# Kernel tuning notes

Hardware: AMD Instinct MI355X
Metric: run time of the kernel (lower is better)

## Reference

```python
import jax, jax.numpy as jnp
import numpy as np

# ---- config (matches init_kwargs) ----
CLIP_FRAMES, CLIP_STRIDE = 1, 2
CODEBOOK_SIZE, CODEBOOK_DIM = 1024, 512
WORD_SIZE = CODEBOOK_SIZE // 4
VOCAB = 3000
LAMBDA_MMD, LAMBDA_SIM = 0.1, 1.0


def conv3d(x, w, b, pad):
    # x: (N,C,T,H,W), w: (O,I,kt,kh,kw)
    out = jax.lax.conv_general_dilated(x, w, (1, 1, 1), [(p, p) for p in pad],
                                       dimension_numbers=('NCDHW', 'OIDHW', 'NCDHW'))
    return out + b[None, :, None, None, None]


def bn_relu(x, g, b, nc):
    # training-mode BatchNorm3d, stats computed per clip-batch (over B,T,H,W),
    # matching the torch loop that calls the encoder once per clip.
    s = x.shape
    xr = x.reshape((nc, s[0] // nc) + s[1:])
    m = xr.mean(axis=(1, 3, 4, 5), keepdims=True)
    v = xr.var(axis=(1, 3, 4, 5), keepdims=True)
    xn = (xr - m) * jax.lax.rsqrt(v + 1e-5)
    xn = xn * g[None, None, :, None, None, None] + b[None, None, :, None, None, None]
    return jax.nn.relu(xn).reshape(s)


def maxpool_hw(x):
    return jax.lax.reduce_window(x, -jnp.inf, jax.lax.max,
                                 (1, 1, 1, 2, 2), (1, 1, 1, 2, 2), 'VALID')


def gru_layer(x, w_ih, w_hh, b_ih, b_hh):
    # PyTorch GRU cell math; x: (B,L,D) -> (B,L,H)
    B = x.shape[0]
    H = w_hh.shape[1]

    def step(h, xt):
        gi = xt @ w_ih.T + b_ih
        gh = h @ w_hh.T + b_hh
        i_r, i_z, i_n = jnp.split(gi, 3, axis=-1)
        h_r, h_z, h_n = jnp.split(gh, 3, axis=-1)
        r = jax.nn.sigmoid(i_r + h_r)
        z = jax.nn.sigmoid(i_z + h_z)
        n = jnp.tanh(i_n + r * h_n)
        hn = (1.0 - z) * n + z * h
        return hn, hn

    h0 = jnp.zeros((B, H), x.dtype)
    _, ys = jax.lax.scan(step, h0, jnp.swapaxes(x, 0, 1))
    return jnp.swapaxes(ys, 0, 1)


def nearest_code(flat, book):
    # squared euclidean distance; argmin identical to torch.cdist(p=2)+argmin
    d2 = (flat * flat).sum(-1, keepdims=True) - 2.0 * flat @ book.T + (book * book).sum(-1)
    return jnp.argmin(d2, axis=-1)


def _forward(videos, conv1_w, conv1_b, bn1_g, bn1_b, conv2_w, conv2_b, bn2_g, bn2_b,
             conv3_w, conv3_b, bn3_g, bn3_b, tconv_w, tconv_b, bn4_g, bn4_b,
             proj_w, proj_b, codebook, word_codebook, align_w, align_b,
             gru_wih0, gru_whh0, gru_bih0, gru_bhh0, gru_wih1, gru_whh1, gru_bih1, gru_bhh1,
             dec1_w, dec1_b, dec2_w, dec2_b, dec3_w, dec3_b, text_tokens):
    sg = jax.lax.stop_gradient
    B, _, T, Hh, Ww = videos.shape
    nc = (T - CLIP_FRAMES) // CLIP_STRIDE + 1
    # gather all clips, fold clip dim into batch for the convs
    idx = jnp.arange(nc)[:, None] * CLIP_STRIDE + jnp.arange(CLIP_FRAMES)[None]
    clips = jnp.transpose(videos[:, :, idx], (2, 0, 1, 3, 4, 5))  # (nc,B,3,cf,H,W)
    x = clips.reshape(nc * B, 3, CLIP_FRAMES, Hh, Ww)
    x = maxpool_hw(bn_relu(conv3d(x, conv1_w, conv1_b, (1, 1, 1)), bn1_g, bn1_b, nc))
    x = maxpool_hw(bn_relu(conv3d(x, conv2_w, conv2_b, (1, 1, 1)), bn2_g, bn2_b, nc))
    x = bn_relu(conv3d(x, conv3_w, conv3_b, (1, 1, 1)), bn3_g, bn3_b, nc)
    # AdaptiveAvgPool3d((CLIP_FRAMES,4,4)): T already CLIP_FRAMES, H,W divisible by 4
    N, C, Tc, Hc, Wc = x.shape
    x = x.reshape(N, C, Tc, 4, Hc // 4, 4, Wc // 4).mean(axis=(4, 6))
    x = bn_relu(conv3d(x, tconv_w, tconv_b, (1, 0, 0)), bn4_g, bn4_b, nc)
    feats = jnp.transpose(x.reshape(nc, B, -1), (1, 0, 2))  # (B, nc, 256*cf*16)
    features = feats @ proj_w.T + proj_b                     # (B, nc, D)
    D = features.shape[-1]
    # --- VQ quantize ---
    flat = features.reshape(-1, D)
    tok = nearest_code(flat, codebook)
    quantized = codebook[tok].reshape(B, nc, D)
    commitment = jnp.mean((features - sg(quantized)) ** 2)
    codebook_loss = jnp.mean((quantized - sg(features)) ** 2)
    h = gru_layer(quantized[:, :-1], gru_wih0, gru_whh0, gru_bih0, gru_bhh0)
    h = gru_layer(h, gru_wih1, gru_whh1, gru_bih1, gru_bhh1)
    context_loss = jnp.mean((h - features[:, 1:]) ** 2)
    vq_loss = commitment + 0.25 * codebook_loss + 0.1 * context_loss
    # --- SimpleCRA: mean of char pairs -> nearest word code ---
    wsrc = quantized.reshape(B, nc // 2, 2, D).mean(axis=2)
    widx = nearest_code(wsrc.reshape(-1, D), word_codebook).reshape(B, nc // 2)
    wemb = word_codebook[widx]  # (B, nw, D)
    flat_w = wemb.reshape(-1, D)
    alignment = jnp.mean((flat_w @ align_w.T + align_b - sg(flat_w)) ** 2)
    # --- translation: mean word context -> MLP decoder -> CE vs first token, summed over batch ---
    ctx = wemb.mean(axis=1)  # (B, D)
    hh = jax.nn.relu(ctx @ dec1_w.T + dec1_b)
    hh = jax.nn.relu(hh @ dec2_w.T + dec2_b)  # dropout = identity (eval)
    logits = hh @ dec3_w.T + dec3_b           # (B, VOCAB)
    logp = jax.nn.log_softmax(logits, axis=-1)
    translation = -jnp.take_along_axis(logp, text_tokens[:, :1], axis=1).sum()
    total = vq_loss + LAMBDA_MMD * alignment + LAMBDA_SIM * translation
    return widx, total


def setup_inputs() -> dict:
    key = jax.random.key(0)
    ks = iter(jax.random.split(key, 48))

    def rn(shape, scale):
        return jax.random.normal(next(ks), shape, jnp.float32) * scale

    D = CODEBOOK_DIM
    inp = {}
    inp['videos'] = jax.random.normal(next(ks), (4, 3, 32, 64, 64), jnp.float32)
    inp['conv1_w'] = rn((64, 3, 3, 3, 3), 0.15); inp['conv1_b'] = jnp.zeros((64,), jnp.float32)
    inp['bn1_g'] = jnp.ones((64,), jnp.float32); inp['bn1_b'] = jnp.zeros((64,), jnp.float32)
    inp['conv2_w'] = rn((128, 64, 3, 3, 3), 0.034); inp['conv2_b'] = jnp.zeros((128,), jnp.float32)
    inp['bn2_g'] = jnp.ones((128,), jnp.float32); inp['bn2_b'] = jnp.zeros((128,), jnp.float32)
    inp['conv3_w'] = rn((256, 128, 3, 3, 3), 0.024); inp['conv3_b'] = jnp.zeros((256,), jnp.float32)
    inp['bn3_g'] = jnp.ones((256,), jnp.float32); inp['bn3_b'] = jnp.zeros((256,), jnp.float32)
    inp['tconv_w'] = rn((256, 256, 3, 1, 1), 0.05); inp['tconv_b'] = jnp.zeros((256,), jnp.float32)
    inp['bn4_g'] = jnp.ones((256,), jnp.float32); inp['bn4_b'] = jnp.zeros((256,), jnp.float32)
    inp['proj_w'] = rn((D, 256 * CLIP_FRAMES * 16), 0.02); inp['proj_b'] = jnp.zeros((D,), jnp.float32)
    inp['codebook'] = jax.random.uniform(next(ks), (CODEBOOK_SIZE, D), jnp.float32,
                                         -1.0 / CODEBOOK_SIZE, 1.0 / CODEBOOK_SIZE)
    inp['word_codebook'] = jax.random.uniform(next(ks), (WORD_SIZE, D), jnp.float32,
                                              -1.0 / WORD_SIZE, 1.0 / WORD_SIZE)
    inp['align_w'] = rn((D, D), 0.04); inp['align_b'] = jnp.zeros((D,), jnp.float32)
    for l in (0, 1):
        inp[f'gru_wih{l}'] = rn((3 * D, D), 0.044)
        inp[f'gru_whh{l}'] = rn((3 * D, D), 0.044)
        inp[f'gru_bih{l}'] = jnp.zeros((3 * D,), jnp.float32)
        inp[f'gru_bhh{l}'] = jnp.zeros((3 * D,), jnp.float32)
    inp['dec1_w'] = rn((512, D), 0.044); inp['dec1_b'] = jnp.zeros((512,), jnp.float32)
    inp['dec2_w'] = rn((1024, 512), 0.044); inp['dec2_b'] = jnp.zeros((1024,), jnp.float32)
    inp['dec3_w'] = rn((VOCAB, 1024), 0.031); inp['dec3_b'] = jnp.zeros((VOCAB,), jnp.float32)
    inp['text_tokens'] = jax.random.randint(next(ks), (4, 10), 0, VOCAB)
    return inp


def reference(videos, conv1_w, conv1_b, bn1_g, bn1_b, conv2_w, conv2_b, bn2_g, bn2_b,
              conv3_w, conv3_b, bn3_g, bn3_b, tconv_w, tconv_b, bn4_g, bn4_b,
              proj_w, proj_b, codebook, word_codebook, align_w, align_b,
              gru_wih0, gru_whh0, gru_bih0, gru_bhh0, gru_wih1, gru_whh1, gru_bih1, gru_bhh1,
              dec1_w, dec1_b, dec2_w, dec2_b, dec3_w, dec3_b, text_tokens):
    return _forward(videos, conv1_w, conv1_b, bn1_g, bn1_b, conv2_w, conv2_b, bn2_g, bn2_b,
                    conv3_w, conv3_b, bn3_g, bn3_b, tconv_w, tconv_b, bn4_g, bn4_b,
                    proj_w, proj_b, codebook, word_codebook, align_w, align_b,
                    gru_wih0, gru_whh0, gru_bih0, gru_bhh0, gru_wih1, gru_whh1, gru_bih1, gru_bhh1,
                    dec1_w, dec1_b, dec2_w, dec2_b, dec3_w, dec3_b, text_tokens)
```

## Files before the change

### kernel.cpp

```cpp
#include <hip/hip_runtime.h>


static const size_t OFF_X1P  = 0;
static const size_t OFF_Y2   = 4194304;
static const size_t OFF_X2P  = 0;
static const size_t OFF_Y3   = 4194304;
static const size_t OFF_X3P  = 2097152;
static const size_t OFF_Y4   = 2359296;
static const size_t OFF_X4   = 2621440;
static const size_t OFF_FEAT = 2883584;
static const size_t OFF_QUANT= 2916352;
static const size_t OFF_GI1  = 2949120;
static const size_t OFF_GI2  = 3047424;
static const size_t OFF_H1   = 3145728;
static const size_t OFF_H2   = 3178496;
static const size_t OFF_WEMB = 3211264;
static const size_t OFF_CTX  = 3227648;
static const size_t OFF_HH1  = 3229696;
static const size_t OFF_HH2  = 3231744;
static const size_t OFF_LOG  = 3235840;
static const size_t OFF_PP   = 3247840;
static const size_t OFF_SC    = 12582912;
static const size_t OFF_SH    = 12587008;
static const size_t OFF_ACCP  = 12591104;
static const size_t OFF_COMMIT= 12623872;
static const size_t OFF_CTXA  = 12623936;
static const size_t OFF_ALIGNA= 12624056;

__global__ __launch_bounds__(256) void k_conv1_stats3(
        const float* __restrict__ videos, const float* __restrict__ w1,
        const float* __restrict__ b1, float* __restrict__ accP) {
    __shared__ float sP[3 * 18 * 66];
    __shared__ float wsm[3 * 9 * 16];
    __shared__ float sRed[4][16], qRed[4][16];
    int oc0 = blockIdx.x * 16, rq = blockIdx.y, n = blockIdx.z;
    int c = n >> 2, b = n & 3;
    int tid = threadIdx.x;
    int rp = tid >> 5, cq = tid & 31;
    for (int e = tid; e < 3564; e += 256) {
        int ic = e / 1188, rem = e % 1188;
        int r = rem / 66, col = rem % 66;
        int gr = rq * 16 - 1 + r, gc = col - 1;
        float v = 0.f;
        if (gr >= 0 && gr < 64 && gc >= 0 && gc < 64)
            v = videos[((size_t)(b * 3 + ic) * 32 + 2 * c) * 4096 + gr * 64 + gc];
        sP[e] = v;
    }
    for (int e = tid; e < 432; e += 256) {
        int ic = e / 144, rem = e % 144, k = rem / 16, j = rem % 16;
        wsm[e] = w1[((size_t)((oc0 + j) * 3 + ic) * 3 + 1) * 9 + k];
    }
    __syncthreads();
    float acc[4][16];
#pragma unroll
    for (int p = 0; p < 4; ++p)
#pragma unroll
        for (int j = 0; j < 16; ++j) acc[p][j] = 0.f;
#pragma unroll
    for (int ic = 0; ic < 3; ++ic) {
        const float* base = &sP[ic * 1188 + (2 * rp) * 66 + 2 * cq];
        float patch[4][4];
#pragma unroll
        for (int r = 0; r < 4; ++r)
#pragma unroll
            for (int q = 0; q < 4; ++q) patch[r][q] = base[r * 66 + q];
#pragma unroll
        for (int k = 0; k < 9; ++k) {
            int kr = k / 3, kc = k % 3;
            float4 w0 = *(const float4*)&wsm[(ic * 9 + k) * 16 + 0];
            float4 w1v = *(const float4*)&wsm[(ic * 9 + k) * 16 + 4];
            float4 w2 = *(const float4*)&wsm[(ic * 9 + k) * 16 + 8];
            float4 w3 = *(const float4*)&wsm[(ic * 9 + k) * 16 + 12];
#pragma unroll
            for (int p = 0; p < 4; ++p) {
                float vv = patch[(p >> 1) + kr][(p & 1) + kc];
                acc[p][0]  += vv * w0.x; acc[p][1]  += vv * w0.y;
                acc[p][2]  += vv * w0.z; acc[p][3]  += vv * w0.w;
                acc[p][4]  += vv * w1v.x; acc[p][5]  += vv * w1v.y;
                acc[p][6]  += vv * w1v.z; acc[p][7]  += vv * w1v.w;
                acc[p][8]  += vv * w2.x; acc[p][9]  += vv * w2.y;
                acc[p][10] += vv * w2.z; acc[p][11] += vv * w2.w;
                acc[p][12] += vv * w3.x; acc[p][13] += vv * w3.y;
                acc[p][14] += vv * w3.z; acc[p][15] += vv * w3.w;
            }
        }
    }
    int lane = tid & 63, wave = tid >> 6;
#pragma unroll
    for (int j = 0; j < 16; ++j) {
        float bj = b1[oc0 + j];
        float s = 0.f, q = 0.f;
#pragma unroll
        for (int p = 0; p < 4; ++p) {
            float a = acc[p][j] + bj;
            s += a; q += a * a;
        }
#pragma unroll
        for (int m = 1; m < 64; m <<= 1) {
            s += __shfl_xor(s, m);
            q += __shfl_xor(q, m);
        }
        if (lane == 0) { sRed[wave][j] = s; qRed[wave][j] = q; }
    }
    __syncthreads();
    if (tid < 16) {
        float s = ((sRed[0][tid] + sRed[1][tid]) + (sRed[2][tid] + sRed[3][tid]));
        float q = ((qRed[0][tid] + qRed[1][tid]) + (qRed[2][tid] + qRed[3][tid]));
        int oc = oc0 + tid;
        size_t slot = (((size_t)(c * 64 + oc)) * 4 + b) * 4 + rq;
        accP[slot] = s;
        accP[16384 + slot] = q;
    }
}

__global__ void k_conv1_fin(const float* __restrict__ accP, const float* __restrict__ g1,
                            const float* __restrict__ be1, float* __restrict__ sc,
                            float* __restrict__ sh) {
    int e = blockIdx.x * 256 + threadIdx.x;
    if (e >= 1024) return;
    int oc = e & 63;
    const float* ps = accP + (size_t)e * 16;
    const float* pq = accP + 16384 + (size_t)e * 16;
    float s = 0.f, q = 0.f;
#pragma unroll
    for (int i = 0; i < 16; ++i) { s += ps[i]; q += pq[i]; }
    float m = s * (1.f / 16384.f);
    float var = q * (1.f / 16384.f) - m * m;
    float sf = g1[oc] * rsqrtf(var + 1e-5f);
    sc[e] = sf;
    sh[e] = be1[oc] - m * sf;
}

__global__ __launch_bounds__(256) void k_conv1_apply3(
        const float* __restrict__ videos, const float* __restrict__ w1,
        const float* __restrict__ b1, const float* __restrict__ sc,
        const float* __restrict__ sh, float* __restrict__ x1p) {
    __shared__ float sP[3 * 18 * 66];
    __shared__ float wsm[3 * 9 * 16];
    int oc0 = blockIdx.x * 16, rq = blockIdx.y, n = blockIdx.z;
    int c = n >> 2, b = n & 3;
    int tid = threadIdx.x;
    int rp = tid >> 5, cq = tid & 31;
    for (int e = tid; e < 3564; e += 256) {
        int ic = e / 1188, rem = e % 1188;
        int r = rem / 66, col = rem % 66;
        int gr = rq * 16 - 1 + r, gc = col - 1;
        float v = 0.f;
        if (gr >= 0 && gr < 64 && gc >= 0 && gc < 64)
            v = videos[((size_t)(b * 3 + ic) * 32 + 2 * c) * 4096 + gr * 64 + gc];
        sP[e] = v;
    }
    for (int e = tid; e < 432; e += 256) {
        int ic = e / 144, rem = e % 144, k = rem / 16, j = rem % 16;
        wsm[e] = w1[((size_t)((oc0 + j) * 3 + ic) * 3 + 1) * 9 + k];
    }
    __syncthreads();
    float acc[4][16];
#pragma unroll
    for (int p = 0; p < 4; ++p)
#pragma unroll
        for (int j = 0; j < 16; ++j) acc[p][j] = 0.f;
#pragma unroll
    for (int ic = 0; ic < 3; ++ic) {
        const float* base = &sP[ic * 1188 + (2 * rp) * 66 + 2 * cq];
        float patch[4][4];
#pragma unroll
        for (int r = 0; r < 4; ++r)
#pragma unroll
            for (int q = 0; q < 4; ++q) patch[r][q] = base[r * 66 + q];
#pragma unroll
        for (int k = 0; k < 9; ++k) {
            int kr = k / 3, kc = k % 3;
            float4 w0 = *(const float4*)&wsm[(ic * 9 + k) * 16 + 0];
            float4 w1v = *(const float4*)&wsm[(ic * 9 + k) * 16 + 4];
            float4 w2 = *(const float4*)&wsm[(ic * 9 + k) * 16 + 8];
            float4 w3 = *(const float4*)&wsm[(ic * 9 + k) * 16 + 12];
#pragma unroll
            for (int p = 0; p < 4; ++p) {
                float vv = patch[(p >> 1) + kr][(p & 1) + kc];
                acc[p][0]  += vv * w0.x; acc[p][1]  += vv * w0.y;
                acc[p][2]  += vv * w0.z; acc[p][3]  += vv * w0.w;
                acc[p][4]  += vv * w1v.x; acc[p][5]  += vv * w1v.y;
                acc[p][6]  += vv * w1v.z; acc[p][7]  += vv * w1v.w;
                acc[p][8]  += vv * w2.x; acc[p][9]  += vv * w2.y;
                acc[p][10] += vv * w2.z; acc[p][11] += vv * w2.w;
                acc[p][12] += vv * w3.x; acc[p][13] += vv * w3.y;
                acc[p][14] += vv * w3.z; acc[p][15] += vv * w3.w;
            }
        }
    }
#pragma unroll
    for (int j = 0; j < 16; ++j) {
        int oc = oc0 + j;
        float bj = b1[oc];
        float scj = sc[c * 64 + oc], shj = sh[c * 64 + oc];
        float m = -1e30f;
#pragma unroll
        for (int p = 0; p < 4; ++p) m = fmaxf(m, (acc[p][j] + bj) * scj + shj);
        x1p[((size_t)n * 64 + oc) * 1024 + (rq * 8 + rp) * 32 + cq] = fmaxf(m, 0.f);
    }
}

__global__ __launch_bounds__(256) void k_conv2(
        const float* __restrict__ in, const float* __restrict__ wt,
        const float* __restrict__ bias, float* __restrict__ out) {
    __shared__ __align__(16) float sIn[8 * 10 * 36];
    __shared__ __align__(16) float sW[8 * 9 * 32];
    int oc0 = blockIdx.x * 32, r0 = blockIdx.y * 8, n = blockIdx.z;
    int tid = threadIdx.x;
    int ocq = tid >> 5;
    int rg = (tid >> 3) & 3;
    int cg = tid & 7;
    float acc[4][8];
#pragma unroll
    for (int j = 0; j < 4; ++j)
#pragma unroll
        for (int p = 0; p < 8; ++p) acc[j][p] = 0.f;

    for (int ic0 = 0; ic0 < 64; ic0 += 8) {
        __syncthreads();
        for (int e = tid; e < 2720; e += 256) {
            int ch = e / 340, rem = e % 340;
            int r = rem / 34, col = rem % 34;
            int gr = r0 - 1 + r, gc = col - 1;
            float v = 0.f;
            if (gr >= 0 && gr < 32 && gc >= 0 && gc < 32)
                v = in[((size_t)(n * 64 + ic0 + ch) * 32 + gr) * 32 + gc];
            sIn[ch * 360 + r * 36 + col] = v;
        }
        for (int e = tid; e < 2304; e += 256) {
            int c = e / 288, r1 = e % 288, k = r1 / 32, j = r1 % 32;
            sW[e] = wt[((size_t)(oc0 + j) * 64 + ic0 + c) * 27 + 9 + k];
        }
        __syncthreads();
        for (int c = 0; c < 8; ++c) {
            const float* base = &sIn[c * 360 + (2 * rg) * 36 + 4 * cg];
            float patch[4][6];
#pragma unroll
            for (int r = 0; r < 4; ++r) {
                float4 p4 = *(const float4*)&base[r * 36];
                float2 p2 = *(const float2*)&base[r * 36 + 4];
                patch[r][0] = p4.x; patch[r][1] = p4.y; patch[r][2] = p4.z;
                patch[r][3] = p4.w; patch[r][4] = p2.x; patch[r][5] = p2.y;
            }
#pragma unroll
            for (int k = 0; k < 9; ++k) {
                int kr = k / 3, kc = k % 3;
                float4 w4 = *(const float4*)&sW[c * 288 + k * 32 + ocq * 4];
#pragma unroll
                for (int p = 0; p < 8; ++p) {
                    int pr = p >> 2, pcq = p & 3;
                    float vv = patch[pr + kr][pcq + kc];
                    acc[0][p] += vv * w4.x; acc[1][p] += vv * w4.y;
                    acc[2][p] += vv * w4.z; acc[3][p] += vv * w4.w;
                }
            }
        }
    }
#pragma unroll
    for (int j = 0; j < 4; ++j) {
        int oc = oc0 + ocq * 4 + j;
        float bj = bias[oc];
#pragma unroll
        for (int pr = 0; pr < 2; ++pr) {
            float4 o4 = make_float4(acc[j][pr * 4 + 0] + bj, acc[j][pr * 4 + 1] + bj,
                                    acc[j][pr * 4 + 2] + bj, acc[j][pr * 4 + 3] + bj);
            *(float4*)&out[((size_t)(n * 128 + oc) * 32 + r0 + 2 * rg + pr) * 32 + 4 * cg] = o4;
        }
    }
}

__global__ __launch_bounds__(256) void k_conv3k(
        const float* __restrict__ in, const float* __restrict__ wt,
        const float* __restrict__ bias, float* __restrict__ out) {
    __shared__ __align__(16) float sIn[8 * 18 * 20];
    __shared__ __align__(16) float sW[8 * 9 * 32];
    int oc0 = blockIdx.x * 32, n = blockIdx.y;
    int tid = threadIdx.x;
    int ocq = tid >> 5;
    int rg = (tid >> 2) & 7;
    int cg = tid & 3;
    float acc[4][8];
#pragma unroll
    for (int j = 0; j < 4; ++j)
#pragma unroll
        for (int p = 0; p < 8; ++p) acc[j][p] = 0.f;

    for (int ic0 = 0; ic0 < 128; ic0 += 8) {
        __syncthreads();
        for (int e = tid; e < 2592; e += 256) {
            int ch = e / 324, rem = e % 324;
            int r = rem / 18, cc = rem % 18;
            int gr = r - 1, gc = cc - 1;
            float v = 0.f;
            if (gr >= 0 && gr < 16 && gc >= 0 && gc < 16)
                v = in[((size_t)(n * 128 + ic0 + ch) * 16 + gr) * 16 + gc];
            sIn[ch * 360 + r * 20 + cc] = v;
        }
        for (int e = tid; e < 2304; e += 256) {
            int c = e / 288, r1 = e % 288, k = r1 / 32, j = r1 % 32;
            sW[e] = wt[((size_t)(oc0 + j) * 128 + ic0 + c) * 27 + 9 + k];
        }
        __syncthreads();
        for (int c = 0; c < 8; ++c) {
            const float* base = &sIn[c * 360 + (2 * rg) * 20 + 4 * cg];
            float patch[4][6];
#pragma unroll
            for (int r = 0; r < 4; ++r) {
                float4 p4 = *(const float4*)&base[r * 20];
                float2 p2 = *(const float2*)&base[r * 20 + 4];
                patch[r][0] = p4.x; patch[r][1] = p4.y; patch[r][2] = p4.z;
                patch[r][3] = p4.w; patch[r][4] = p2.x; patch[r][5] = p2.y;
            }
#pragma unroll
            for (int k = 0; k < 9; ++k) {
                int kr = k / 3, kc = k % 3;
                float4 w4 = *(const float4*)&sW[c * 288 + k * 32 + ocq * 4];
#pragma unroll
                for (int p = 0; p < 8; ++p) {
                    int pr = p >> 2, pcq = p & 3;
                    float vv = patch[pr + kr][pcq + kc];
                    acc[0][p] += vv * w4.x; acc[1][p] += vv * w4.y;
                    acc[2][p] += vv * w4.z; acc[3][p] += vv * w4.w;
                }
            }
        }
    }
#pragma unroll
    for (int j = 0; j < 4; ++j) {
        int oc = oc0 + ocq * 4 + j;
        float bj = bias[oc];
#pragma unroll
        for (int pr = 0; pr < 2; ++pr) {
            float4 o4 = make_float4(acc[j][pr * 4 + 0] + bj, acc[j][pr * 4 + 1] + bj,
                                    acc[j][pr * 4 + 2] + bj, acc[j][pr * 4 + 3] + bj);
            *(float4*)&out[((size_t)(n * 256 + oc) * 16 + 2 * rg + pr) * 16 + 4 * cg] = o4;
        }
    }
}

__global__ void k_bn_stats(const float* __restrict__ buf, const float* __restrict__ g,
                           const float* __restrict__ be, float* __restrict__ scale,
                           float* __restrict__ shift, int C, int HW) {
    int c = blockIdx.x, ch = blockIdx.y, tid = threadIdx.x;
    float s = 0.f, s2 = 0.f;
    for (int b = 0; b < 4; ++b) {
        const float* p = buf + ((size_t)(c * 4 + b) * C + ch) * HW;
        for (int i = tid; i < HW; i += 256) { float v = p[i]; s += v; s2 += v * v; }
    }
    __shared__ float rs[256], rq[256];
    rs[tid] = s; rq[tid] = s2; __syncthreads();
    for (int k = 128; k > 0; k >>= 1) {
        if (tid < k) { rs[tid] += rs[tid + k]; rq[tid] += rq[tid + k]; }
        __syncthreads();
    }
    if (tid == 0) {
        float inv = 1.f / (float)(4 * HW);
        float m = rs[0] * inv, var = rq[0] * inv - m * m;
        float sc = g[ch] * rsqrtf(var + 1e-5f);
        scale[c * C + ch] = sc;
        shift[c * C + ch] = be[ch] - m * sc;
    }
}

__global__ void k_bn_apply_pool(const float* __restrict__ in, const float* __restrict__ scale,
                                const float* __restrict__ shift, float* __restrict__ out,
                                int C, int H, int W) {
    int OH = H >> 1, OW = W >> 1;
    size_t idx = (size_t)blockIdx.x * 256 + threadIdx.x;
    int ow = (int)(idx % OW);
    size_t r = idx / OW;
    int oh = (int)(r % OH); r /= OH;
    int ch = (int)(r % C);
    int n = (int)(r / C);
    int c = n >> 2;
    float sc = scale[c * C + ch], sh = shift[c * C + ch];
    const float* p = in + (((size_t)n * C + ch) * H + 2 * oh) * W + 2 * ow;
    float m = 0.f;
    m = fmaxf(m, p[0] * sc + sh);
    m = fmaxf(m, p[1] * sc + sh);
    m = fmaxf(m, p[W] * sc + sh);
    m = fmaxf(m, p[W + 1] * sc + sh);
    out[idx] = m;
}

__global__ void k_bn_apply_avgpool4(const float* __restrict__ in, const float* __restrict__ scale,
                                    const float* __restrict__ shift, float* __restrict__ out) {
    size_t idx = (size_t)blockIdx.x * 256 + threadIdx.x;
    int j = (int)(idx & 3), i = (int)(idx >> 2) & 3;
    int ch = (int)(idx >> 4) & 255, n = (int)(idx >> 12);
    int c = n >> 2;
    float sc = scale[c * 256 + ch], sh = shift[c * 256 + ch];
    const float* p = in + (((size_t)n * 256 + ch) * 16 + i * 4) * 16 + j * 4;
    float s = 0.f;
#pragma unroll
    for (int r = 0; r < 4; ++r)
#pragma unroll
        for (int q = 0; q < 4; ++q) s += fmaxf(p[r * 16 + q] * sc + sh, 0.f);
    out[idx] = s * (1.f / 16.f);
}

__global__ void k_tconv(const float* __restrict__ x3p, const float* __restrict__ tw,
                        const float* __restrict__ tb, float* __restrict__ y4) {
    size_t idx = (size_t)blockIdx.x * 256 + threadIdx.x;
    int p = (int)(idx & 15), o = (int)(idx >> 4) & 255, n = (int)(idx >> 12);
    const float* xr = x3p + (size_t)n * 4096 + p;
    float a = tb[o];
    for (int i = 0; i < 256; ++i) a += xr[i * 16] * tw[((size_t)o * 256 + i) * 3 + 1];
    y4[idx] = a;
}

__global__ void k_bn_apply(const float* __restrict__ in, const float* __restrict__ scale,
                           const float* __restrict__ shift, float* __restrict__ out) {
    size_t idx = (size_t)blockIdx.x * 256 + threadIdx.x;
    int ch = (int)(idx >> 4) & 255, n = (int)(idx >> 12);
    int c = n >> 2;
    float sc = scale[c * 256 + ch], sh = shift[c * 256 + ch];
    out[idx] = fmaxf(in[idx] * sc + sh, 0.f);
}

__global__ __launch_bounds__(256) void k_proj_part(
        const float* __restrict__ A, const float* __restrict__ B, float* __restrict__ PP) {
    __shared__ __align__(16) float As[64 * 68];
    __shared__ __align__(16) float Bs[64 * 68];
    int n0 = blockIdx.x * 64, ks = blockIdx.y;
    int tid = threadIdx.x, tm = tid >> 4, tn = tid & 15;
    float acc[4][4];
#pragma unroll
    for (int i = 0; i < 4; ++i)
#pragma unroll
        for (int j = 0; j < 4; ++j) acc[i][j] = 0.f;
    int kb = ks * 512;
    for (int k0 = kb; k0 < kb + 512; k0 += 64) {
        __syncthreads();
        for (int e = tid; e < 4096; e += 256) {
            int m = e >> 6, k = e & 63;
            As[k * 68 + m] = A[(size_t)m * 4096 + k0 + k];
            Bs[k * 68 + m] = B[(size_t)(n0 + m) * 4096 + k0 + k];
        }
        __syncthreads();
        for (int k = 0; k < 64; ++k) {
            float4 a4 = *(const float4*)&As[k * 68 + tm * 4];
            float4 b4 = *(const float4*)&Bs[k * 68 + tn * 4];
            acc[0][0] += a4.x * b4.x; acc[0][1] += a4.x * b4.y;
            acc[0][2] += a4.x * b4.z; acc[0][3] += a4.x * b4.w;
            acc[1][0] += a4.y * b4.x; acc[1][1] += a4.y * b4.y;
            acc[1][2] += a4.y * b4.z; acc[1][3] += a4.y * b4.w;
            acc[2][0] += a4.z * b4.x; acc[2][1] += a4.z * b4.y;
            acc[2][2] += a4.z * b4.z; acc[2][3] += a4.z * b4.w;
            acc[3][0] += a4.w * b4.x; acc[3][1] += a4.w * b4.y;
            acc[3][2] += a4.w * b4.z; acc[3][3] += a4.w * b4.w;
        }
    }
#pragma unroll
    for (int i = 0; i < 4; ++i)
#pragma unroll
        for (int j = 0; j < 4; ++j)
            PP[((size_t)(ks * 64 + tm * 4 + i)) * 512 + n0 + tn * 4 + j] = acc[i][j];
}

__global__ void k_proj_fin(const float* __restrict__ PP, const float* __restrict__ pb,
                           float* __restrict__ feat) {
    int e = blockIdx.x * 256 + threadIdx.x;
    int n = e & 511;
    int m = e >> 9;
    float s = pb[n];
#pragma unroll
    for (int ks = 0; ks < 8; ++ks) s += PP[(size_t)ks * 32768 + e];
    int c = m >> 2, b = m & 3;
    int ro = b * 16 + c;
    feat[(size_t)ro * 512 + n] = s;
}

__global__ void k_vq(const float* __restrict__ feat, const float* __restrict__ cb,
                     float* __restrict__ quant, float* __restrict__ commitArr) {
    int row = blockIdx.x, tid = threadIdx.x;
    __shared__ float f[512];
    for (int k = tid; k < 512; k += 256) f[k] = feat[(size_t)row * 512 + k];
    __syncthreads();
    float best = 3.4e38f; int bidx = 0;
    for (int j = tid; j < 1024; j += 256) {
        const float* c = cb + (size_t)j * 512;
        float d2 = 0.f;
        for (int k = 0; k < 512; ++k) { float t = f[k] - c[k]; d2 += t * t; }
        if (d2 < best) { best = d2; bidx = j; }
    }
    __shared__ float rd[256]; __shared__ int ri[256];
    rd[tid] = best; ri[tid] = bidx; __syncthreads();
    for (int k = 128; k > 0; k >>= 1) {
        if (tid < k) {
            float od = rd[tid + k]; int oi = ri[tid + k];
            if (od < rd[tid] || (od == rd[tid] && oi < ri[tid])) { rd[tid] = od; ri[tid] = oi; }
        }
        __syncthreads();
    }
    __shared__ int wsel;
    if (tid == 0) { wsel = ri[0]; commitArr[row] = rd[0]; }
    __syncthreads();
    const float* c = cb + (size_t)wsel * 512;
    for (int k = tid; k < 512; k += 256) quant[(size_t)row * 512 + k] = c[k];
}

__global__ void k_gru_gi(const float* __restrict__ x, const float* __restrict__ wih,
                         const float* __restrict__ bih, float* __restrict__ gi) {
    int r = blockIdx.x;
    int b = r / 15, t = r % 15;
    const float* xr = x + ((size_t)(b * 16 + t)) * 512;
    __shared__ float xsRow[512];
    for (int k = threadIdx.x; k < 512; k += 256) xsRow[k] = xr[k];
    __syncthreads();
    const float4* xp = (const float4*)xsRow;
    for (int d = threadIdx.x; d < 1536; d += 256) {
        const float4* wr = (const float4*)(wih + (size_t)d * 512);
        float a0 = 0.f, a1 = 0.f, a2 = 0.f, a3 = 0.f;
        for (int i = 0; i < 128; i += 4) {
            float4 w0 = wr[i], w1 = wr[i + 1], w2 = wr[i + 2], w3 = wr[i + 3];
            float4 x0 = xp[i], x1 = xp[i + 1], x2 = xp[i + 2], x3 = xp[i + 3];
            a0 += w0.x * x0.x + w0.y * x0.y + w0.z * x0.z + w0.w * x0.w;
            a1 += w1.x * x1.x + w1.y * x1.y + w1.z * x1.z + w1.w * x1.w;
            a2 += w2.x * x2.x + w2.y * x2.y + w2.z * x2.z + w2.w * x2.w;
            a3 += w3.x * x3.x + w3.y * x3.y + w3.z * x3.z + w3.w * x3.w;
        }
        gi[((size_t)(b * 16 + t)) * 1536 + d] = (a0 + a1) + (a2 + a3) + bih[d];
    }
}

__global__ void k_gru_step2(const float* __restrict__ gi, const float* __restrict__ whh,
                            const float* __restrict__ bhh, float* __restrict__ hseq, int t) {
    int wv = threadIdx.x >> 6, lane = threadIdx.x & 63;
    int d = blockIdx.x * 4 + wv;
    const float4* w0p = (const float4*)(whh + (size_t)d * 512);
    const float4* w1p = (const float4*)(whh + (size_t)(512 + d) * 512);
    const float4* w2p = (const float4*)(whh + (size_t)(1024 + d) * 512);
    float4 w0a = w0p[lane * 2], w0b = w0p[lane * 2 + 1];
    float4 w1a = w1p[lane * 2], w1b = w1p[lane * 2 + 1];
    float4 w2a = w2p[lane * 2], w2b = w2p[lane * 2 + 1];
    float bh0 = bhh[d], bh1 = bhh[512 + d], bh2 = bhh[1024 + d];
    for (int b = 0; b < 4; ++b) {
        float4 ha = make_float4(0, 0, 0, 0), hb = ha;
        float hpd = 0.f;
        if (t > 0) {
            const float4* hp = (const float4*)(hseq + (size_t)(b * 16 + t - 1) * 512);
            ha = hp[lane * 2]; hb = hp[lane * 2 + 1];
            hpd = hseq[(size_t)(b * 16 + t - 1) * 512 + d];
        }
        float s0 = w0a.x * ha.x + w0a.y * ha.y + w0a.z * ha.z + w0a.w * ha.w
                 + w0b.x * hb.x + w0b.y * hb.y + w0b.z * hb.z + w0b.w * hb.w;
        float s1 = w1a.x * ha.x + w1a.y * ha.y + w1a.z * ha.z + w1a.w * ha.w
                 + w1b.x * hb.x + w1b.y * hb.y + w1b.z * hb.z + w1b.w * hb.w;
        float s2 = w2a.x * ha.x + w2a.y * ha.y + w2a.z * ha.z + w2a.w * ha.w
                 + w2b.x * hb.x + w2b.y * hb.y + w2b.z * hb.z + w2b.w * hb.w;
#pragma unroll
        for (int m = 1; m < 64; m <<= 1) {
            s0 += __shfl_xor(s0, m);
            s1 += __shfl_xor(s1, m);
            s2 += __shfl_xor(s2, m);
        }
        const float* gr = gi + (size_t)(b * 16 + t) * 1536;
        float rr = 1.f / (1.f + expf(-(gr[d] + s0 + bh0)));
        float zz = 1.f / (1.f + expf(-(gr[512 + d] + s1 + bh1)));
        float nn = tanhf(gr[1024 + d] + rr * (s2 + bh2));
        if (lane == 0)
            hseq[(size_t)(b * 16 + t) * 512 + d] = (1.f - zz) * nn + zz * hpd;
    }
}

__global__ void k_ctx_loss(const float* __restrict__ h2, const float* __restrict__ feat,
                           float* __restrict__ ctxArr) {
    int tid = threadIdx.x;
    size_t idx = (size_t)blockIdx.x * 256 + tid;
    int d = (int)(idx & 511);
    int rt = (int)(idx >> 9);
    int t = rt % 15, b = rt / 15;
    float diff = h2[(size_t)(b * 16 + t) * 512 + d] - feat[(size_t)(b * 16 + t + 1) * 512 + d];
    float v = diff * diff;
#pragma unroll
    for (int m = 1; m < 64; m <<= 1) v += __shfl_xor(v, m);
    __shared__ float ws[4];
    if ((tid & 63) == 0) ws[tid >> 6] = v;
    __syncthreads();
    if (tid == 0) ctxArr[blockIdx.x] = ((ws[0] + ws[1]) + (ws[2] + ws[3]));
}

__global__ void k_word_vq(const float* __restrict__ quant, const float* __restrict__ wcb,
                          float* __restrict__ wemb, float* __restrict__ out_widx) {
    int row = blockIdx.x;
    int b = row >> 3, wi = row & 7;
    int tid = threadIdx.x;
    __shared__ float f[512];
    for (int k = tid; k < 512; k += 256)
        f[k] = 0.5f * (quant[(size_t)(b * 16 + 2 * wi) * 512 + k] +
                       quant[(size_t)(b * 16 + 2 * wi + 1) * 512 + k]);
    __syncthreads();
    const float* cp = wcb + (size_t)tid * 512;
    float d2 = 0.f;
    for (int k = 0; k < 512; ++k) { float t = f[k] - cp[k]; d2 += t * t; }
    __shared__ float rd[256]; __shared__ int ri[256];
    rd[tid] = d2; ri[tid] = tid; __syncthreads();
    for (int k = 128; k > 0; k >>= 1) {
        if (tid < k) {
            float od = rd[tid + k]; int oi = ri[tid + k];
            if (od < rd[tid] || (od == rd[tid] && oi < ri[tid])) { rd[tid] = od; ri[tid] = oi; }
        }
        __syncthreads();
    }
    __shared__ int wsel;
    if (tid == 0) { wsel = ri[0]; out_widx[row] = (float)ri[0]; }
    __syncthreads();
    const float* cb = wcb + (size_t)wsel * 512;
    for (int k = tid; k < 512; k += 256) wemb[(size_t)row * 512 + k] = cb[k];
}

__global__ void k_align(const float* __restrict__ wemb, const float* __restrict__ aw,
                        const float* __restrict__ ab, float* __restrict__ alignArr) {
    int row = blockIdx.x, tid = threadIdx.x;
    __shared__ float e[512];
    for (int k = tid; k < 512; k += 256) e[k] = wemb[(size_t)row * 512 + k];
    __syncthreads();
    float local = 0.f;
    for (int d = tid; d < 512; d += 256) {
        const float* wr = aw + (size_t)d * 512;
        float a = ab[d] - e[d];
        for (int k = 0; k < 512; ++k) a += e[k] * wr[k];
        local += a * a;
    }
    __shared__ float rs[256];
    rs[tid] = local; __syncthreads();
    for (int k = 128; k > 0; k >>= 1) { if (tid < k) rs[tid] += rs[tid + k]; __syncthreads(); }
    if (tid == 0) alignArr[row] = rs[0];
}

__global__ void k_ctx(const float* __restrict__ wemb, float* __restrict__ ctx) {
    int e = blockIdx.x * 256 + threadIdx.x;
    int b = e >> 9, d = e & 511;
    float s = 0.f;
#pragma unroll
    for (int wi = 0; wi < 8; ++wi) s += wemb[(size_t)(b * 8 + wi) * 512 + d];
    ctx[e] = s * 0.125f;
}

__global__ void k_smallM(const float* __restrict__ A, const float* __restrict__ B,
                         const float* __restrict__ bias, float* __restrict__ C,
                         int N, int K, int relu) {
    __shared__ float xs[4096];
    int tid = threadIdx.x;
    for (int e = tid; e < 4 * K; e += 256) xs[e] = A[e];
    __syncthreads();
    int r = tid >> 4, kt = tid & 15;
    int n = blockIdx.x * 16 + r;
    float acc[4] = {0, 0, 0, 0};
    if (n < N) {
        int iters = K >> 6;
        for (int i = 0; i < iters; ++i) {
            int k = i * 64 + kt * 4;
            float4 w = *(const float4*)&B[(size_t)n * K + k];
#pragma unroll
            for (int b = 0; b < 4; ++b) {
                float4 x = *(const float4*)&xs[b * K + k];
                acc[b] += w.x * x.x + w.y * x.y + w.z * x.z + w.w * x.w;
            }
        }
    }
#pragma unroll
    for (int b = 0; b < 4; ++b) {
#pragma unroll
        for (int m = 1; m < 16; m <<= 1) acc[b] += __shfl_xor(acc[b], m);
    }
    if (kt == 0 && n < N) {
#pragma unroll
        for (int b = 0; b < 4; ++b) {
            float v = acc[b] + bias[n];
            if (relu) v = fmaxf(v, 0.f);
            C[(size_t)b * N + n] = v;
        }
    }
}

__global__ void k_final(const float* __restrict__ logits, const int* __restrict__ tokens,
                        const float* __restrict__ commitArr, const float* __restrict__ ctxArr,
                        const float* __restrict__ alignArr, float* __restrict__ out_total) {
    int tid = threadIdx.x;
    __shared__ float rs[256];
    __shared__ float sM;
    float tr = 0.f;
    for (int b = 0; b < 4; ++b) {
        const float* lg = logits + (size_t)b * 3000;
        float m = -1e30f;
        for (int d = tid; d < 3000; d += 256) m = fmaxf(m, lg[d]);
        rs[tid] = m; __syncthreads();
        for (int k = 128; k > 0; k >>= 1) { if (tid < k) rs[tid] = fmaxf(rs[tid], rs[tid + k]); __syncthreads(); }
        if (tid == 0) sM = rs[0];
        __syncthreads();
        float M = sM;
        float s = 0.f;
        for (int d = tid; d < 3000; d += 256) s += expf(lg[d] - M);
        rs[tid] = s; __syncthreads();
        for (int k = 128; k > 0; k >>= 1) { if (tid < k) rs[tid] += rs[tid + k]; __syncthreads(); }
        if (tid == 0) {
            int t0 = tokens[b * 10];
            tr += -(lg[t0] - M - logf(rs[0]));
        }
        __syncthreads();
    }
    if (tid == 0) {
        float c0 = 0.f;
        for (int i = 0; i < 64; ++i) c0 += commitArr[i];
        float c1 = 0.f;
        for (int i = 0; i < 120; ++i) c1 += ctxArr[i];
        float c2 = 0.f;
        for (int i = 0; i < 32; ++i) c2 += alignArr[i];
        float total = 1.25f * c0 * (1.f / 32768.f)
                    + 0.1f  * c1 * (1.f / 30720.f)
                    + 0.1f  * c2 * (1.f / 16384.f)
                    + tr;
        *out_total = total;
    }
}

extern "C" void kernel_launch(void* const* d_in, const int* in_sizes, int n_in,
                              void* d_out, int out_size, void* d_ws, size_t ws_size,
                              hipStream_t stream) {
    (void)in_sizes; (void)n_in; (void)out_size; (void)ws_size;
    const float* videos   = (const float*)d_in[0];
    const float* conv1_w  = (const float*)d_in[1];
    const float* conv1_b  = (const float*)d_in[2];
    const float* bn1_g    = (const float*)d_in[3];
    const float* bn1_b    = (const float*)d_in[4];
    const float* conv2_w  = (const float*)d_in[5];
    const float* conv2_b  = (const float*)d_in[6];
    const float* bn2_g    = (const float*)d_in[7];
    const float* bn2_b    = (const float*)d_in[8];
    const float* conv3_w  = (const float*)d_in[9];
    const float* conv3_b  = (const float*)d_in[10];
    const float* bn3_g    = (const float*)d_in[11];
    const float* bn3_b    = (const float*)d_in[12];
    const float* tconv_w  = (const float*)d_in[13];
    const float* tconv_b  = (const float*)d_in[14];
    const float* bn4_g    = (const float*)d_in[15];
    const float* bn4_b    = (const float*)d_in[16];
    const float* proj_w   = (const float*)d_in[17];
    const float* proj_b   = (const float*)d_in[18];
    const float* codebook = (const float*)d_in[19];
    const float* word_cb  = (const float*)d_in[20];
    const float* align_w  = (const float*)d_in[21];
    const float* align_b  = (const float*)d_in[22];
    const float* gru_wih0 = (const float*)d_in[23];
    const float* gru_whh0 = (const float*)d_in[24];
    const float* gru_bih0 = (const float*)d_in[25];
    const float* gru_bhh0 = (const float*)d_in[26];
    const float* gru_wih1 = (const float*)d_in[27];
    const float* gru_whh1 = (const float*)d_in[28];
    const float* gru_bih1 = (const float*)d_in[29];
    const float* gru_bhh1 = (const float*)d_in[30];
    const float* dec1_w   = (const float*)d_in[31];
    const float* dec1_b   = (const float*)d_in[32];
    const float* dec2_w   = (const float*)d_in[33];
    const float* dec2_b   = (const float*)d_in[34];
    const float* dec3_w   = (const float*)d_in[35];
    const float* dec3_b   = (const float*)d_in[36];
    const int*   tokens   = (const int*)d_in[37];

    float* wsf    = (float*)d_ws;
    float* out    = (float*)d_out;
    float* x1p    = wsf + OFF_X1P;
    float* x2p    = wsf + OFF_X2P;
    float* y2     = wsf + OFF_Y2;
    float* y3     = wsf + OFF_Y3;
    float* x3p    = wsf + OFF_X3P;
    float* y4     = wsf + OFF_Y4;
    float* x4     = wsf + OFF_X4;
    float* feat   = wsf + OFF_FEAT;
    float* quant  = wsf + OFF_QUANT;
    float* gi1    = wsf + OFF_GI1;
    float* gi2    = wsf + OFF_GI2;
    float* h1     = wsf + OFF_H1;
    float* h2     = wsf + OFF_H2;
    float* wemb   = wsf + OFF_WEMB;
    float* ctx    = wsf + OFF_CTX;
    float* hh1    = wsf + OFF_HH1;
    float* hh2    = wsf + OFF_HH2;
    float* logit  = wsf + OFF_LOG;
    float* pp     = wsf + OFF_PP;
    float* sc     = wsf + OFF_SC;
    float* sh     = wsf + OFF_SH;
    float* accP   = wsf + OFF_ACCP;
    float* commitA= wsf + OFF_COMMIT;
    float* ctxA   = wsf + OFF_CTXA;
    float* alignA = wsf + OFF_ALIGNA;

    k_conv1_stats3<<<dim3(4, 4, 64), 256, 0, stream>>>(videos, conv1_w, conv1_b, accP);
    k_conv1_fin<<<4, 256, 0, stream>>>(accP, bn1_g, bn1_b, sc, sh);
    k_conv1_apply3<<<dim3(4, 4, 64), 256, 0, stream>>>(videos, conv1_w, conv1_b, sc, sh, x1p);
    k_conv2<<<dim3(4, 4, 64), 256, 0, stream>>>(x1p, conv2_w, conv2_b, y2);
    k_bn_stats<<<dim3(16, 128), 256, 0, stream>>>(y2, bn2_g, bn2_b, sc, sh, 128, 1024);
    k_bn_apply_pool<<<8192, 256, 0, stream>>>(y2, sc, sh, x2p, 128, 32, 32);
    k_conv3k<<<dim3(8, 64), 256, 0, stream>>>(x2p, conv3_w, conv3_b, y3);
    k_bn_stats<<<dim3(16, 256), 256, 0, stream>>>(y3, bn3_g, bn3_b, sc, sh, 256, 256);
    k_bn_apply_avgpool4<<<1024, 256, 0, stream>>>(y3, sc, sh, x3p);
    k_tconv<<<1024, 256, 0, stream>>>(x3p, tconv_w, tconv_b, y4);
    k_bn_stats<<<dim3(16, 256), 256, 0, stream>>>(y4, bn4_g, bn4_b, sc, sh, 256, 16);
    k_bn_apply<<<1024, 256, 0, stream>>>(y4, sc, sh, x4);
    k_proj_part<<<dim3(8, 8), 256, 0, stream>>>(x4, proj_w, pp);
    k_proj_fin<<<128, 256, 0, stream>>>(pp, proj_b, feat);
    k_vq<<<64, 256, 0, stream>>>(feat, codebook, quant, commitA);
    k_gru_gi<<<60, 256, 0, stream>>>(quant, gru_wih0, gru_bih0, gi1);
    for (int t = 0; t < 15; ++t)
        k_gru_step2<<<128, 256, 0, stream>>>(gi1, gru_whh0, gru_bhh0, h1, t);
    k_gru_gi<<<60, 256, 0, stream>>>(h1, gru_wih1, gru_bih1, gi2);
    for (int t = 0; t < 15; ++t)
        k_gru_step2<<<128, 256, 0, stream>>>(gi2, gru_whh1, gru_bhh1, h2, t);
    k_ctx_loss<<<120, 256, 0, stream>>>(h2, feat, ctxA);
    k_word_vq<<<32, 256, 0, stream>>>(quant, word_cb, wemb, out);
    k_align<<<32, 256, 0, stream>>>(wemb, align_w, align_b, alignA);
    k_ctx<<<8, 256, 0, stream>>>(wemb, ctx);
    k_smallM<<<32, 256, 0, stream>>>(ctx, dec1_w, dec1_b, hh1, 512, 512, 1);
    k_smallM<<<64, 256, 0, stream>>>(hh1, dec2_w, dec2_b, hh2, 1024, 512, 1);
    k_smallM<<<188, 256, 0, stream>>>(hh2, dec3_w, dec3_b, logit, 3000, 1024, 0);
    k_final<<<1, 256, 0, stream>>>(logit, tokens, commitA, ctxA, alignA, out + 32);
}
```

Before: 1.182 ms.

## Pipeline two GRU layers as a wavefront across timesteps in one kernel

Layer 1's input projection and layer 2's recurrent step are interleaved with layer 1's steps in a single per-timestep kernel using disjoint block ranges. Layer 2 runs two steps behind, so the launch count drops from 32 to 17. The first input-projection kernel is also split six ways across 360 blocks to spread the 1536 outputs over more CUs. The catch is that correctness relies on the block ranges within each launch touching independent timesteps, and each launch now carries more work.

```diff
diff --git a/kernel.cpp b/kernel.cpp
--- a/kernel.cpp
+++ b/kernel.cpp
@@ -501,34 +501,28 @@
     for (int k = tid; k < 512; k += 256) quant[(size_t)row * 512 + k] = c[k];
 }
 
-__global__ void k_gru_gi(const float* __restrict__ x, const float* __restrict__ wih,
-                         const float* __restrict__ bih, float* __restrict__ gi) {
-    int r = blockIdx.x;
-    int b = r / 15, t = r % 15;
-    const float* xr = x + ((size_t)(b * 16 + t)) * 512;
-    __shared__ float xsRow[512];
-    for (int k = threadIdx.x; k < 512; k += 256) xsRow[k] = xr[k];
-    __syncthreads();
+__device__ __forceinline__ void gru_gi_one(
+        const float* __restrict__ xsRow, const float* __restrict__ wih,
+        const float* __restrict__ bih, float* __restrict__ gi, int row, int d) {
     const float4* xp = (const float4*)xsRow;
-    for (int d = threadIdx.x; d < 1536; d += 256) {
-        const float4* wr = (const float4*)(wih + (size_t)d * 512);
-        float a0 = 0.f, a1 = 0.f, a2 = 0.f, a3 = 0.f;
-        for (int i = 0; i < 128; i += 4) {
-            float4 w0 = wr[i], w1 = wr[i + 1], w2 = wr[i + 2], w3 = wr[i + 3];
-            float4 x0 = xp[i], x1 = xp[i + 1], x2 = xp[i + 2], x3 = xp[i + 3];
-            a0 += w0.x * x0.x + w0.y * x0.y + w0.z * x0.z + w0.w * x0.w;
-            a1 += w1.x * x1.x + w1.y * x1.y + w1.z * x1.z + w1.w * x1.w;
-            a2 += w2.x * x2.x + w2.y * x2.y + w2.z * x2.z + w2.w * x2.w;
-            a3 += w3.x * x3.x + w3.y * x3.y + w3.z * x3.z + w3.w * x3.w;
-        }
-        gi[((size_t)(b * 16 + t)) * 1536 + d] = (a0 + a1) + (a2 + a3) + bih[d];
-    }
-}
-
-__global__ void k_gru_step2(const float* __restrict__ gi, const float* __restrict__ whh,
-                            const float* __restrict__ bhh, float* __restrict__ hseq, int t) {
+    const float4* wr = (const float4*)(wih + (size_t)d * 512);
+    float a0 = 0.f, a1 = 0.f, a2 = 0.f, a3 = 0.f;
+    for (int i = 0; i < 128; i += 4) {
+        float4 w0 = wr[i], w1 = wr[i + 1], w2 = wr[i + 2], w3 = wr[i + 3];
+        float4 x0 = xp[i], x1 = xp[i + 1], x2 = xp[i + 2], x3 = xp[i + 3];
+        a0 += w0.x * x0.x + w0.y * x0.y + w0.z * x0.z + w0.w * x0.w;
+        a1 += w1.x * x1.x + w1.y * x1.y + w1.z * x1.z + w1.w * x1.w;
+        a2 += w2.x * x2.x + w2.y * x2.y + w2.z * x2.z + w2.w * x2.w;
+        a3 += w3.x * x3.x + w3.y * x3.y + w3.z * x3.z + w3.w * x3.w;
+    }
+    gi[(size_t)row * 1536 + d] = (a0 + a1) + (a2 + a3) + bih[d];
+}
+
+__device__ __forceinline__ void gru_step_body(
+        const float* __restrict__ gi, const float* __restrict__ whh,
+        const float* __restrict__ bhh, float* __restrict__ hseq, int t, int blk) {
     int wv = threadIdx.x >> 6, lane = threadIdx.x & 63;
-    int d = blockIdx.x * 4 + wv;
+    int d = blk * 4 + wv;
     const float4* w0p = (const float4*)(whh + (size_t)d * 512);
     const float4* w1p = (const float4*)(whh + (size_t)(512 + d) * 512);
     const float4* w2p = (const float4*)(whh + (size_t)(1024 + d) * 512);
@@ -562,6 +556,43 @@
         float nn = tanhf(gr[1024 + d] + rr * (s2 + bh2));
         if (lane == 0)
             hseq[(size_t)(b * 16 + t) * 512 + d] = (1.f - zz) * nn + zz * hpd;
+    }
+}
+
+__global__ void k_gru_gi6(const float* __restrict__ x, const float* __restrict__ wih,
+                          const float* __restrict__ bih, float* __restrict__ gi) {
+    int g = blockIdx.x;
+    int r = g / 6, part = g % 6;
+    int b = r / 15, t = r % 15;
+    int row = b * 16 + t;
+    __shared__ float xsRow[512];
+    for (int k = threadIdx.x; k < 512; k += 256) xsRow[k] = x[(size_t)row * 512 + k];
+    __syncthreads();
+    gru_gi_one(xsRow, wih, bih, gi, row, part * 256 + threadIdx.x);
+}
+
+__global__ __launch_bounds__(256) void k_gru_pipe(
+        const float* __restrict__ gi1, const float* __restrict__ whh0,
+        const float* __restrict__ bhh0, float* __restrict__ h1,
+        const float* __restrict__ wih1, const float* __restrict__ bih1,
+        float* __restrict__ gi2, const float* __restrict__ whh1,
+        const float* __restrict__ bhh1, float* __restrict__ h2, int t) {
+    int bid = blockIdx.x;
+    if (bid < 128) {
+        if (t < 15) gru_step_body(gi1, whh0, bhh0, h1, t, bid);
+    } else if (bid < 256) {
+        if (t >= 2) gru_step_body(gi2, whh1, bhh1, h2, t - 2, bid - 128);
+    } else {
+        if (t >= 1 && t <= 15) {
+            int local = bid - 256;
+            int b = local / 6, part = local % 6;
+            int row = b * 16 + (t - 1);
+            __shared__ float xsRow[512];
+            for (int k = threadIdx.x; k < 512; k += 256)
+                xsRow[k] = h1[(size_t)row * 512 + k];
+            __syncthreads();
+            gru_gi_one(xsRow, wih1, bih1, gi2, row, part * 256 + threadIdx.x);
+        }
     }
 }
 
@@ -803,12 +834,11 @@
     k_proj_part<<<dim3(8, 8), 256, 0, stream>>>(x4, proj_w, pp);
     k_proj_fin<<<128, 256, 0, stream>>>(pp, proj_b, feat);
     k_vq<<<64, 256, 0, stream>>>(feat, codebook, quant, commitA);
-    k_gru_gi<<<60, 256, 0, stream>>>(quant, gru_wih0, gru_bih0, gi1);
-    for (int t = 0; t < 15; ++t)
-        k_gru_step2<<<128, 256, 0, stream>>>(gi1, gru_whh0, gru_bhh0, h1, t);
-    k_gru_gi<<<60, 256, 0, stream>>>(h1, gru_wih1, gru_bih1, gi2);
-    for (int t = 0; t < 15; ++t)
-        k_gru_step2<<<128, 256, 0, stream>>>(gi2, gru_whh1, gru_bhh1, h2, t);
+    k_gru_gi6<<<360, 256, 0, stream>>>(quant, gru_wih0, gru_bih0, gi1);
+    for (int t = 0; t <= 16; ++t)
+        k_gru_pipe<<<280, 256, 0, stream>>>(gi1, gru_whh0, gru_bhh0, h1,
+                                            gru_wih1, gru_bih1, gi2,
+                                            gru_whh1, gru_bhh1, h2, t);
     k_ctx_loss<<<120, 256, 0, stream>>>(h2, feat, ctxA);
     k_word_vq<<<32, 256, 0, stream>>>(quant, word_cb, wemb, out);
     k_align<<<32, 256, 0, stream>>>(wemb, align_w, align_b, alignA);
```

Result: faster. 1.118 ms (-5.4%).
